# Kernel tuning notes

Hardware: AMD Instinct MI355X
Metric: run time of the kernel (lower is better)

The kernel has to match this reference:

```python
import jax, jax.numpy as jnp
import numpy as np

N0, T0, T1 = 3514368, 135168, 12288   # hop-0 nodes, layer-0 targets, layer-1 targets
F0, F1 = 25, 10                        # sampled fanouts per layer
D, H, C = 100, 256, 128                # in_feat, hidden, class_count
IC = 4096                              # id_count (src/pos/neg each)


def setup_inputs() -> dict:
    key = jax.random.key(0)
    ks = jax.random.split(key, 16)

    def w(k, shape):
        return jax.random.normal(k, shape, dtype=jnp.float32) * (1.0 / np.sqrt(shape[0]))

    x_feat = jax.random.normal(ks[0], (N0, D), dtype=jnp.float32)
    col_ind0 = jax.random.randint(ks[1], (T0, F0), 0, N0)
    col_ind1 = jax.random.randint(ks[2], (T1, F1), 0, T0)
    reverse_map = jax.random.randint(ks[3], (3 * IC,), 0, T1)

    return {
        "x_feat": x_feat,
        "Wn0": w(ks[4], (D, H)), "Ws0": w(ks[5], (D, H)), "b0": jnp.zeros((H,), jnp.float32),
        "Wn1": w(ks[6], (H, C)), "Ws1": w(ks[7], (H, C)), "b1": jnp.zeros((C,), jnp.float32),
        "Wp1": w(ks[8], (C, C)), "bp1": jnp.zeros((C,), jnp.float32),
        "Wp2": w(ks[9], (C, 1)), "bp2": jnp.zeros((1,), jnp.float32),
        "col_ind0": col_ind0, "col_ind1": col_ind1, "reverse_map": reverse_map,
        "id_count": IC,
    }


def reference(x_feat, Wn0, Ws0, b0, Wn1, Ws1, b1, Wp1, bp1, Wp2, bp2,
              col_ind0, col_ind1, reverse_map, id_count):
    t0 = col_ind0.shape[0]
    t1 = col_ind1.shape[0]

    # SAGEConv layer 0 (mean aggregator): gather neighbor feats, mean over fanout
    neigh0 = x_feat[col_ind0].mean(axis=1)                    # [t0, D]
    h = neigh0 @ Wn0 + x_feat[:t0] @ Ws0 + b0                 # [t0, H]
    h = jax.nn.relu(h)                                        # dropout p=0 (eval)

    # SAGEConv layer 1 -> class_count, no activation on final layer
    neigh1 = h[col_ind1].mean(axis=1)                         # [t1, H]
    out_unique = neigh1 @ Wn1 + h[:t1] @ Ws1 + b1             # [t1, C]

    # embedding gather of unique outputs back to (src, pos_dst, neg_dst) order
    out_feat = out_unique[reverse_map]                        # [3*ic, C]
    src = out_feat[:id_count]
    pos = out_feat[id_count:2 * id_count]
    neg = out_feat[2 * id_count:3 * id_count]

    h_src = jnp.concatenate([src, src], axis=0)               # [2*ic, C]
    h_dst = jnp.concatenate([pos, neg], axis=0)               # [2*ic, C]

    # edge predictor: MLP on elementwise product -> scalar score
    e = h_src * h_dst
    scores = jax.nn.relu(e @ Wp1 + bp1) @ Wp2 + bp2           # [2*ic, 1]
    return scores
```

## Files before the change

kernel.cpp:

```cpp
#include <hip/hip_runtime.h>
#include <hip/hip_bf16.h>

#define N0_ 3514368
#define T0_ 135168
#define T1_ 12288
#define F0_ 25
#define F1_ 10
#define D_  100
#define H_  256
#define C_  128
#define IC_ 4096


typedef __attribute__((ext_vector_type(8))) short bf8_t;
typedef __attribute__((ext_vector_type(4))) float f4_t;

__device__ inline void split_bf16(float v, ushort& hi, ushort& lo) {
    __hip_bfloat16 hb = __float2bfloat16(v);
    float hf = __bfloat162float(hb);
    __hip_bfloat16 lb = __float2bfloat16(v - hf);
    hi = *reinterpret_cast<ushort*>(&hb);
    lo = *reinterpret_cast<ushort*>(&lb);
}

__global__ __launch_bounds__(256) void bz_zero(unsigned int* __restrict__ flag32) {
    const int i = blockIdx.x * 256 + threadIdx.x;
    if (i < T0_ / 4) flag32[i] = 0u;
}

__global__ __launch_bounds__(256) void bs_set(const int* __restrict__ col1,
                                              unsigned char* __restrict__ flag) {
    const int i = blockIdx.x * 256 + threadIdx.x;
    if (i < T1_ * F1_) flag[col1[i]] = 1;
    if (i < T1_) flag[i] = 1;
}

__global__ __launch_bounds__(256) void k0_packW(const float* __restrict__ Wn0,
                                                const float* __restrict__ Ws0,
                                                ushort* __restrict__ Wpk) {
    const int nb = blockIdx.x;
    for (int it = 0; it < 4; ++it) {
        const int task = threadIdx.x + it * 256;
        const int ks   = task >> 7;
        const int part = (task >> 6) & 1;
        const int lane = task & 63;
        const int n  = nb * 16 + (lane & 15);
        const int kb = (ks & 3) * 32 + (lane >> 4) * 8;
        const float* src = (ks < 4) ? Wn0 : Ws0;
        ushort out[8];
#pragma unroll
        for (int j = 0; j < 8; ++j) {
            const int k = kb + j;
            float v = (k < D_) ? src[k * H_ + n] : 0.f;
            ushort hi, lo;
            split_bf16(v, hi, lo);
            out[j] = part ? lo : hi;
        }
        ushort* dst = Wpk + ((size_t)((nb * 8 + ks) * 2 + part) * 64 + lane) * 8;
        *reinterpret_cast<bf8_t*>(dst) = *reinterpret_cast<bf8_t*>(out);
    }
}

__global__ __launch_bounds__(256) void k12_fused(const float* __restrict__ xf,
                                                 const int* __restrict__ col0,
                                                 const ushort* __restrict__ Wpk,
                                                 const float* __restrict__ b0,
                                                 const unsigned char* __restrict__ flag,
                                                 float* __restrict__ h) {
    __shared__ ushort Afr[4][8][2][512];
    const int lane = threadIdx.x & 63;
    const int wid  = threadIdx.x >> 6;
    const int r    = lane & 15;
    const int kg   = lane >> 4;
    const size_t row = (size_t)blockIdx.x * 64 + wid * 16 + r;
    const bool needed = (flag[row] != 0);

    float accN[4][8];
    float accS[4][8];
#pragma unroll
    for (int ks = 0; ks < 4; ++ks)
#pragma unroll
        for (int j = 0; j < 8; ++j) { accN[ks][j] = 0.f; accS[ks][j] = 0.f; }

    if (needed) {
        const int* cp = col0 + row * F0_;
#pragma unroll 5
        for (int jn = 0; jn < F0_; ++jn) {
            const float* rp = xf + (size_t)cp[jn] * D_;
#pragma unroll
            for (int ks = 0; ks < 3; ++ks) {
                float4 a = *reinterpret_cast<const float4*>(rp + ks * 32 + kg * 8);
                float4 b = *reinterpret_cast<const float4*>(rp + ks * 32 + kg * 8 + 4);
                accN[ks][0] += a.x; accN[ks][1] += a.y; accN[ks][2] += a.z; accN[ks][3] += a.w;
                accN[ks][4] += b.x; accN[ks][5] += b.y; accN[ks][6] += b.z; accN[ks][7] += b.w;
            }
            if (kg == 0) {
                float4 a = *reinterpret_cast<const float4*>(rp + 96);
                accN[3][0] += a.x; accN[3][1] += a.y; accN[3][2] += a.z; accN[3][3] += a.w;
            }
        }
        const float* rp = xf + row * D_;
#pragma unroll
        for (int ks = 0; ks < 3; ++ks) {
            float4 a = *reinterpret_cast<const float4*>(rp + ks * 32 + kg * 8);
            float4 b = *reinterpret_cast<const float4*>(rp + ks * 32 + kg * 8 + 4);
            accS[ks][0] = a.x; accS[ks][1] = a.y; accS[ks][2] = a.z; accS[ks][3] = a.w;
            accS[ks][4] = b.x; accS[ks][5] = b.y; accS[ks][6] = b.z; accS[ks][7] = b.w;
        }
        if (kg == 0) {
            float4 a = *reinterpret_cast<const float4*>(rp + 96);
            accS[3][0] = a.x; accS[3][1] = a.y; accS[3][2] = a.z; accS[3][3] = a.w;
        }
    }

    const float inv = 1.0f / F0_;
#pragma unroll
    for (int ks = 0; ks < 4; ++ks) {
        bf8_t hN, lN, hS, lS;
#pragma unroll
        for (int j = 0; j < 8; ++j) {
            ushort hi, lo;
            split_bf16(accN[ks][j] * inv, hi, lo);
            hN[j] = (short)hi; lN[j] = (short)lo;
            split_bf16(accS[ks][j], hi, lo);
            hS[j] = (short)hi; lS[j] = (short)lo;
        }
        *reinterpret_cast<bf8_t*>(&Afr[wid][ks    ][0][lane * 8]) = hN;
        *reinterpret_cast<bf8_t*>(&Afr[wid][ks    ][1][lane * 8]) = lN;
        *reinterpret_cast<bf8_t*>(&Afr[wid][ks + 4][0][lane * 8]) = hS;
        *reinterpret_cast<bf8_t*>(&Afr[wid][ks + 4][1][lane * 8]) = lS;
    }
    __syncthreads();

    const int nb0 = wid * 4;
    f4_t acc[4][4] = {};
#pragma unroll
    for (int ks = 0; ks < 8; ++ks) {
        bf8_t ah[4], al[4], bh[4], bl[4];
#pragma unroll
        for (int rb = 0; rb < 4; ++rb) {
            ah[rb] = *reinterpret_cast<const bf8_t*>(&Afr[rb][ks][0][lane * 8]);
            al[rb] = *reinterpret_cast<const bf8_t*>(&Afr[rb][ks][1][lane * 8]);
        }
#pragma unroll
        for (int ci = 0; ci < 4; ++ci) {
            const ushort* p = Wpk + ((size_t)(((nb0 + ci) * 8 + ks) * 2) * 64 + lane) * 8;
            bh[ci] = *reinterpret_cast<const bf8_t*>(p);
            bl[ci] = *reinterpret_cast<const bf8_t*>(p + 512);
        }
#pragma unroll
        for (int rb = 0; rb < 4; ++rb)
#pragma unroll
            for (int ci = 0; ci < 4; ++ci) {
                acc[rb][ci] = __builtin_amdgcn_mfma_f32_16x16x32_bf16(ah[rb], bh[ci], acc[rb][ci], 0, 0, 0);
                acc[rb][ci] = __builtin_amdgcn_mfma_f32_16x16x32_bf16(ah[rb], bl[ci], acc[rb][ci], 0, 0, 0);
                acc[rb][ci] = __builtin_amdgcn_mfma_f32_16x16x32_bf16(al[rb], bh[ci], acc[rb][ci], 0, 0, 0);
            }
    }

    const int col_in = lane & 15;
    const int rgrp   = lane >> 4;
    bool vflag[4][4];
#pragma unroll
    for (int rb = 0; rb < 4; ++rb)
#pragma unroll
        for (int q = 0; q < 4; ++q)
            vflag[rb][q] = (flag[(size_t)blockIdx.x * 64 + rb * 16 + rgrp * 4 + q] != 0);
#pragma unroll
    for (int ci = 0; ci < 4; ++ci) {
        const int n = (nb0 + ci) * 16 + col_in;
        const float bias = b0[n];
#pragma unroll
        for (int rb = 0; rb < 4; ++rb) {
            const size_t rowb = (size_t)blockIdx.x * 64 + rb * 16 + rgrp * 4;
#pragma unroll
            for (int q = 0; q < 4; ++q) {
                if (vflag[rb][q]) {
                    float v = acc[rb][ci][q] + bias;
                    h[(rowb + q) * H_ + n] = v > 0.f ? v : 0.f;
                }
            }
        }
    }
}

__global__ __launch_bounds__(256) void k3_layer1(const float* __restrict__ h,
                                                 const int* __restrict__ col1,
                                                 const float* __restrict__ Wn1,
                                                 const float* __restrict__ Ws1,
                                                 const float* __restrict__ b1,
                                                 float* __restrict__ out_u) {
    __shared__ __align__(16) float Ng[16 * H_];
    __shared__ __align__(16) float Sf[16 * H_];
    const int t = threadIdx.x;
    const int base = blockIdx.x * 16;

    for (int r = 0; r < 16; ++r) {
        float a = 0.f;
#pragma unroll
        for (int j = 0; j < F1_; ++j) {
            int idx = col1[(base + r) * F1_ + j];
            a += h[(size_t)idx * H_ + t];
        }
        Ng[r * H_ + t] = a * (1.0f / F1_);
        Sf[r * H_ + t] = h[(size_t)(base + r) * H_ + t];
    }
    __syncthreads();

    const int c  = t & (C_ - 1);
    const int rg = t >> 7;
    float acc[8];
    const float bias = b1[c];
#pragma unroll
    for (int r8 = 0; r8 < 8; ++r8) acc[r8] = bias;

    for (int d4 = 0; d4 < H_ / 4; ++d4) {
        const int d = d4 * 4;
        const float wn0_ = Wn1[(d + 0) * C_ + c];
        const float wn1_ = Wn1[(d + 1) * C_ + c];
        const float wn2_ = Wn1[(d + 2) * C_ + c];
        const float wn3_ = Wn1[(d + 3) * C_ + c];
        const float ws0_ = Ws1[(d + 0) * C_ + c];
        const float ws1_ = Ws1[(d + 1) * C_ + c];
        const float ws2_ = Ws1[(d + 2) * C_ + c];
        const float ws3_ = Ws1[(d + 3) * C_ + c];
#pragma unroll
        for (int r8 = 0; r8 < 8; ++r8) {
            const int r = rg * 8 + r8;
            float4 n = *reinterpret_cast<const float4*>(&Ng[r * H_ + d]);
            float4 s = *reinterpret_cast<const float4*>(&Sf[r * H_ + d]);
            acc[r8] += n.x * wn0_ + n.y * wn1_ + n.z * wn2_ + n.w * wn3_
                     + s.x * ws0_ + s.y * ws1_ + s.z * ws2_ + s.w * ws3_;
        }
    }
#pragma unroll
    for (int r8 = 0; r8 < 8; ++r8)
        out_u[(size_t)(base + rg * 8 + r8) * C_ + c] = acc[r8];
}

__global__ __launch_bounds__(256) void k4_edges(const float* __restrict__ out_u,
                                                const int* __restrict__ rmap,
                                                const float* __restrict__ Wp1,
                                                const float* __restrict__ bp1,
                                                const float* __restrict__ Wp2,
                                                const float* __restrict__ bp2,
                                                float* __restrict__ scores) {
    __shared__ __align__(16) float E[32 * C_];
    const int t = threadIdx.x;
    const int base = blockIdx.x * 32;
    const int f = t & 127;
    const int half = t >> 7;

    for (int rr = 0; rr < 16; ++rr) {
        const int row = rr * 2 + half;
        const int j = base + row;
        const int si = rmap[j & (IC_ - 1)];
        const int di = rmap[IC_ + j];
        E[row * C_ + f] = out_u[(size_t)si * C_ + f] * out_u[(size_t)di * C_ + f];
    }
    __syncthreads();

    float acc[16];
    const float bias = bp1[f];
#pragma unroll
    for (int r16 = 0; r16 < 16; ++r16) acc[r16] = bias;

    for (int d4 = 0; d4 < C_ / 4; ++d4) {
        const int d = d4 * 4;
        const float w0 = Wp1[(d + 0) * C_ + f];
        const float w1 = Wp1[(d + 1) * C_ + f];
        const float w2 = Wp1[(d + 2) * C_ + f];
        const float w3 = Wp1[(d + 3) * C_ + f];
#pragma unroll
        for (int r16 = 0; r16 < 16; ++r16) {
            const int r = half * 16 + r16;
            float4 e4 = *reinterpret_cast<const float4*>(&E[r * C_ + d]);
            acc[r16] += e4.x * w0 + e4.y * w1 + e4.z * w2 + e4.w * w3;
        }
    }
    __syncthreads();
#pragma unroll
    for (int r16 = 0; r16 < 16; ++r16) {
        float v = acc[r16];
        E[(half * 16 + r16) * C_ + f] = v > 0.f ? v : 0.f;
    }
    __syncthreads();

    const int r = t >> 3;
    const int s = t & 7;
    float p = 0.f;
#pragma unroll
    for (int k4 = 0; k4 < 4; ++k4) {
        float4 tv = *reinterpret_cast<const float4*>(&E[r * C_ + s * 16 + k4 * 4]);
        float4 wv = *reinterpret_cast<const float4*>(&Wp2[s * 16 + k4 * 4]);
        p += tv.x * wv.x + tv.y * wv.y + tv.z * wv.z + tv.w * wv.w;
    }
    p += __shfl_down(p, 4, 8);
    p += __shfl_down(p, 2, 8);
    p += __shfl_down(p, 1, 8);
    if (s == 0) scores[base + r] = p + bp2[0];
}

extern "C" void kernel_launch(void* const* d_in, const int* in_sizes, int n_in,
                              void* d_out, int out_size, void* d_ws, size_t ws_size,
                              hipStream_t stream) {
    const float* xf   = (const float*)d_in[0];
    const float* Wn0  = (const float*)d_in[1];
    const float* Ws0  = (const float*)d_in[2];
    const float* b0   = (const float*)d_in[3];
    const float* Wn1  = (const float*)d_in[4];
    const float* Ws1  = (const float*)d_in[5];
    const float* b1   = (const float*)d_in[6];
    const float* Wp1  = (const float*)d_in[7];
    const float* bp1  = (const float*)d_in[8];
    const float* Wp2  = (const float*)d_in[9];
    const float* bp2  = (const float*)d_in[10];
    const int*   col0 = (const int*)d_in[11];
    const int*   col1 = (const int*)d_in[12];
    const int*   rmap = (const int*)d_in[13];

    char* ws = (char*)d_ws;
    float*  h     = (float*)ws;
    float*  out_u = h + (size_t)T0_ * H_;
    ushort* Wpk   = (ushort*)(out_u + (size_t)T1_ * C_);
    unsigned char* flag = (unsigned char*)(Wpk + (size_t)16 * 8 * 2 * 64 * 8);
    float*  scores = (float*)d_out;

    hipLaunchKernelGGL(bz_zero, dim3((T0_ / 4 + 255) / 256), dim3(256), 0, stream,
                       (unsigned int*)flag);
    hipLaunchKernelGGL(bs_set, dim3((T1_ * F1_ + 255) / 256), dim3(256), 0, stream,
                       col1, flag);
    hipLaunchKernelGGL(k0_packW, dim3(16), dim3(256), 0, stream, Wn0, Ws0, Wpk);
    hipLaunchKernelGGL(k12_fused, dim3(T0_ / 64), dim3(256), 0, stream,
                       xf, col0, Wpk, b0, flag, h);
    hipLaunchKernelGGL(k3_layer1, dim3(T1_ / 16), dim3(256), 0, stream,
                       h, col1, Wn1, Ws1, b1, out_u);
    hipLaunchKernelGGL(k4_edges, dim3((2 * IC_) / 32), dim3(256), 0, stream,
                       out_u, rmap, Wp1, bp1, Wp2, bp2, scores);
}
```

Before: 402.0 us.

## Keep A fragments in registers and loop each wave over all output columns

Drops the shared-memory staging of the bf16 hi/lo A fragments and the block-wide barrier. Each wave now multiplies its own 16 rows against all 16 column blocks of the packed weight, instead of sharing A across waves and computing only 4 column blocks. This removes LDS traffic and the __syncthreads. In exchange, each wave reads four times as much packed weight data from global memory/cache, and the MFMA chain per accumulator is serial with less independent work in flight.

Result: slower. 475.1 us (+18.2%).

```diff
diff --git a/kernel.cpp b/kernel.cpp
--- a/kernel.cpp
+++ b/kernel.cpp
@@ -67,7 +67,6 @@
                                                  const float* __restrict__ b0,
                                                  const unsigned char* __restrict__ flag,
                                                  float* __restrict__ h) {
-    __shared__ ushort Afr[4][8][2][512];
     const int lane = threadIdx.x & 63;
     const int wid  = threadIdx.x >> 6;
     const int r    = lane & 15;
@@ -113,6 +112,7 @@
         }
     }
 
+    bf8_t afH[8], afL[8];
     const float inv = 1.0f / F0_;
 #pragma unroll
     for (int ks = 0; ks < 4; ++ks) {
@@ -125,60 +125,37 @@
             split_bf16(accS[ks][j], hi, lo);
             hS[j] = (short)hi; lS[j] = (short)lo;
         }
-        *reinterpret_cast<bf8_t*>(&Afr[wid][ks    ][0][lane * 8]) = hN;
-        *reinterpret_cast<bf8_t*>(&Afr[wid][ks    ][1][lane * 8]) = lN;
-        *reinterpret_cast<bf8_t*>(&Afr[wid][ks + 4][0][lane * 8]) = hS;
-        *reinterpret_cast<bf8_t*>(&Afr[wid][ks + 4][1][lane * 8]) = lS;
-    }
-    __syncthreads();
-
-    const int nb0 = wid * 4;
-    f4_t acc[4][4] = {};
-#pragma unroll
-    for (int ks = 0; ks < 8; ++ks) {
-        bf8_t ah[4], al[4], bh[4], bl[4];
-#pragma unroll
-        for (int rb = 0; rb < 4; ++rb) {
-            ah[rb] = *reinterpret_cast<const bf8_t*>(&Afr[rb][ks][0][lane * 8]);
-            al[rb] = *reinterpret_cast<const bf8_t*>(&Afr[rb][ks][1][lane * 8]);
-        }
-#pragma unroll
-        for (int ci = 0; ci < 4; ++ci) {
-            const ushort* p = Wpk + ((size_t)(((nb0 + ci) * 8 + ks) * 2) * 64 + lane) * 8;
-            bh[ci] = *reinterpret_cast<const bf8_t*>(p);
-            bl[ci] = *reinterpret_cast<const bf8_t*>(p + 512);
-        }
-#pragma unroll
-        for (int rb = 0; rb < 4; ++rb)
-#pragma unroll
-            for (int ci = 0; ci < 4; ++ci) {
-                acc[rb][ci] = __builtin_amdgcn_mfma_f32_16x16x32_bf16(ah[rb], bh[ci], acc[rb][ci], 0, 0, 0);
-                acc[rb][ci] = __builtin_amdgcn_mfma_f32_16x16x32_bf16(ah[rb], bl[ci], acc[rb][ci], 0, 0, 0);
-                acc[rb][ci] = __builtin_amdgcn_mfma_f32_16x16x32_bf16(al[rb], bh[ci], acc[rb][ci], 0, 0, 0);
-            }
-    }
-
+        afH[ks] = hN; afL[ks] = lN;
+        afH[ks + 4] = hS; afL[ks + 4] = lS;
+    }
+
+    const int rgrp = lane >> 4;
+    bool vflag[4];
+#pragma unroll
+    for (int q = 0; q < 4; ++q)
+        vflag[q] = (flag[(size_t)blockIdx.x * 64 + wid * 16 + rgrp * 4 + q] != 0);
+    const size_t rowb = (size_t)blockIdx.x * 64 + wid * 16 + rgrp * 4;
     const int col_in = lane & 15;
-    const int rgrp   = lane >> 4;
-    bool vflag[4][4];
-#pragma unroll
-    for (int rb = 0; rb < 4; ++rb)
-#pragma unroll
-        for (int q = 0; q < 4; ++q)
-            vflag[rb][q] = (flag[(size_t)blockIdx.x * 64 + rb * 16 + rgrp * 4 + q] != 0);
-#pragma unroll
-    for (int ci = 0; ci < 4; ++ci) {
-        const int n = (nb0 + ci) * 16 + col_in;
+
+#pragma unroll 4
+    for (int nb = 0; nb < 16; ++nb) {
+        f4_t acc = {};
+#pragma unroll
+        for (int ks = 0; ks < 8; ++ks) {
+            const ushort* p = Wpk + ((size_t)((nb * 8 + ks) * 2) * 64 + lane) * 8;
+            bf8_t bh = *reinterpret_cast<const bf8_t*>(p);
+            bf8_t bl = *reinterpret_cast<const bf8_t*>(p + 512);
+            acc = __builtin_amdgcn_mfma_f32_16x16x32_bf16(afH[ks], bh, acc, 0, 0, 0);
+            acc = __builtin_amdgcn_mfma_f32_16x16x32_bf16(afH[ks], bl, acc, 0, 0, 0);
+            acc = __builtin_amdgcn_mfma_f32_16x16x32_bf16(afL[ks], bh, acc, 0, 0, 0);
+        }
+        const int n = nb * 16 + col_in;
         const float bias = b0[n];
 #pragma unroll
-        for (int rb = 0; rb < 4; ++rb) {
-            const size_t rowb = (size_t)blockIdx.x * 64 + rb * 16 + rgrp * 4;
-#pragma unroll
-            for (int q = 0; q < 4; ++q) {
-                if (vflag[rb][q]) {
-                    float v = acc[rb][ci][q] + bias;
-                    h[(rowb + q) * H_ + n] = v > 0.f ? v : 0.f;
-                }
+        for (int q = 0; q < 4; ++q) {
+            if (vflag[q]) {
+                float v = acc[q] + bias;
+                h[(rowb + q) * H_ + n] = v > 0.f ? v : 0.f;
             }
         }
     }
```

## Compact needed layer-0 rows into a list and launch work only for them

Applied to the files above, without the earlier changes.

Adds count/scan/emit kernels that build a compacted list of the layer-0 rows actually referenced by layer 1, and rewrites the fused layer-0 kernel to process rows from this list. Blocks past the count exit early, so unneeded rows no longer occupy MFMA or block slots. Neighbor indices are also preloaded into registers. It adds three small kernel launches, including a serial single-thread scan, and turns the output stores into scattered writes.

Measured after the change: 394.7 us. About the same (-1.8%).

```diff
diff --git a/kernel.cpp b/kernel.cpp
--- a/kernel.cpp
+++ b/kernel.cpp
@@ -10,6 +10,7 @@
 #define H_  256
 #define C_  128
 #define IC_ 4096
+#define CBLK_ 132
 
 
 typedef __attribute__((ext_vector_type(8))) short bf8_t;
@@ -33,6 +34,51 @@
     const int i = blockIdx.x * 256 + threadIdx.x;
     if (i < T1_ * F1_) flag[col1[i]] = 1;
     if (i < T1_) flag[i] = 1;
+}
+
+__global__ __launch_bounds__(1024) void kc_count(const unsigned char* __restrict__ flag,
+                                                 int* __restrict__ counts) {
+    __shared__ int wsum[16];
+    const int i = blockIdx.x * 1024 + threadIdx.x;
+    const int pred = flag[i] ? 1 : 0;
+    unsigned long long b = __ballot(pred);
+    const int lane = threadIdx.x & 63, w = threadIdx.x >> 6;
+    if (lane == 0) wsum[w] = __popcll(b);
+    __syncthreads();
+    if (threadIdx.x == 0) {
+        int s = 0;
+        for (int k = 0; k < 16; ++k) s += wsum[k];
+        counts[blockIdx.x] = s;
+    }
+}
+
+__global__ void kc_scan(const int* __restrict__ counts,
+                        int* __restrict__ offs, int* __restrict__ ntot) {
+    if (threadIdx.x == 0 && blockIdx.x == 0) {
+        int s = 0;
+        for (int k = 0; k < CBLK_; ++k) { offs[k] = s; s += counts[k]; }
+        ntot[0] = s;
+    }
+}
+
+__global__ __launch_bounds__(1024) void kc_emit(const unsigned char* __restrict__ flag,
+                                                const int* __restrict__ offs,
+                                                int* __restrict__ rowlist) {
+    __shared__ int wsum[16];
+    __shared__ int woff[16];
+    const int i = blockIdx.x * 1024 + threadIdx.x;
+    const int pred = flag[i] ? 1 : 0;
+    unsigned long long b = __ballot(pred);
+    const int lane = threadIdx.x & 63, w = threadIdx.x >> 6;
+    const int lanepre = __popcll(b & ((1ULL << lane) - 1ULL));
+    if (lane == 0) wsum[w] = __popcll(b);
+    __syncthreads();
+    if (threadIdx.x == 0) {
+        int s = 0;
+        for (int k = 0; k < 16; ++k) { woff[k] = s; s += wsum[k]; }
+    }
+    __syncthreads();
+    if (pred) rowlist[offs[blockIdx.x] + woff[w] + lanepre] = i;
 }
 
 __global__ __launch_bounds__(256) void k0_packW(const float* __restrict__ Wn0,
@@ -65,15 +111,26 @@
                                                  const int* __restrict__ col0,
                                                  const ushort* __restrict__ Wpk,
                                                  const float* __restrict__ b0,
-                                                 const unsigned char* __restrict__ flag,
+                                                 const int* __restrict__ rowlist,
+                                                 const int* __restrict__ ntot,
                                                  float* __restrict__ h) {
     __shared__ ushort Afr[4][8][2][512];
+    __shared__ int rl[64];
+    const int n = ntot[0];
+    if (blockIdx.x * 64 >= n) return;
+
     const int lane = threadIdx.x & 63;
     const int wid  = threadIdx.x >> 6;
     const int r    = lane & 15;
     const int kg   = lane >> 4;
-    const size_t row = (size_t)blockIdx.x * 64 + wid * 16 + r;
-    const bool needed = (flag[row] != 0);
+    const int cidx = blockIdx.x * 64 + wid * 16 + r;
+    const bool act = (cidx < n);
+    const int orow = rowlist[act ? cidx : 0];
+
+    if (threadIdx.x < 64) {
+        const int c2 = blockIdx.x * 64 + threadIdx.x;
+        rl[threadIdx.x] = (c2 < n) ? rowlist[c2] : -1;
+    }
 
     float accN[4][8];
     float accS[4][8];
@@ -82,11 +139,14 @@
 #pragma unroll
         for (int j = 0; j < 8; ++j) { accN[ks][j] = 0.f; accS[ks][j] = 0.f; }
 
-    if (needed) {
-        const int* cp = col0 + row * F0_;
+    if (act) {
+        const int* cp = col0 + (size_t)orow * F0_;
+        int idxs[F0_];
+#pragma unroll
+        for (int j = 0; j < F0_; ++j) idxs[j] = cp[j];
 #pragma unroll 5
         for (int jn = 0; jn < F0_; ++jn) {
-            const float* rp = xf + (size_t)cp[jn] * D_;
+            const float* rp = xf + (size_t)idxs[jn] * D_;
 #pragma unroll
             for (int ks = 0; ks < 3; ++ks) {
                 float4 a = *reinterpret_cast<const float4*>(rp + ks * 32 + kg * 8);
@@ -99,7 +159,7 @@
                 accN[3][0] += a.x; accN[3][1] += a.y; accN[3][2] += a.z; accN[3][3] += a.w;
             }
         }
-        const float* rp = xf + row * D_;
+        const float* rp = xf + (size_t)orow * D_;
 #pragma unroll
         for (int ks = 0; ks < 3; ++ks) {
             float4 a = *reinterpret_cast<const float4*>(rp + ks * 32 + kg * 8);
@@ -160,24 +220,24 @@
 
     const int col_in = lane & 15;
     const int rgrp   = lane >> 4;
-    bool vflag[4][4];
+    int orows[4][4];
 #pragma unroll
     for (int rb = 0; rb < 4; ++rb)
 #pragma unroll
         for (int q = 0; q < 4; ++q)
-            vflag[rb][q] = (flag[(size_t)blockIdx.x * 64 + rb * 16 + rgrp * 4 + q] != 0);
+            orows[rb][q] = rl[rb * 16 + rgrp * 4 + q];
 #pragma unroll
     for (int ci = 0; ci < 4; ++ci) {
-        const int n = (nb0 + ci) * 16 + col_in;
-        const float bias = b0[n];
+        const int nn = (nb0 + ci) * 16 + col_in;
+        const float bias = b0[nn];
 #pragma unroll
         for (int rb = 0; rb < 4; ++rb) {
-            const size_t rowb = (size_t)blockIdx.x * 64 + rb * 16 + rgrp * 4;
 #pragma unroll
             for (int q = 0; q < 4; ++q) {
-                if (vflag[rb][q]) {
+                const int o = orows[rb][q];
+                if (o >= 0) {
                     float v = acc[rb][ci][q] + bias;
-                    h[(rowb + q) * H_ + n] = v > 0.f ? v : 0.f;
+                    h[(size_t)o * H_ + nn] = v > 0.f ? v : 0.f;
                 }
             }
         }
@@ -324,15 +384,22 @@
     float*  out_u = h + (size_t)T0_ * H_;
     ushort* Wpk   = (ushort*)(out_u + (size_t)T1_ * C_);
     unsigned char* flag = (unsigned char*)(Wpk + (size_t)16 * 8 * 2 * 64 * 8);
-    float*  scores = (float*)d_out;
+    int*    counts  = (int*)(flag + T0_);
+    int*    offs    = counts + CBLK_;
+    int*    ntot    = offs + CBLK_;
+    int*    rowlist = ntot + 1;
+    float*  scores  = (float*)d_out;
 
     hipLaunchKernelGGL(bz_zero, dim3((T0_ / 4 + 255) / 256), dim3(256), 0, stream,
                        (unsigned int*)flag);
     hipLaunchKernelGGL(bs_set, dim3((T1_ * F1_ + 255) / 256), dim3(256), 0, stream,
                        col1, flag);
+    hipLaunchKernelGGL(kc_count, dim3(CBLK_), dim3(1024), 0, stream, flag, counts);
+    hipLaunchKernelGGL(kc_scan, dim3(1), dim3(64), 0, stream, counts, offs, ntot);
+    hipLaunchKernelGGL(kc_emit, dim3(CBLK_), dim3(1024), 0, stream, flag, offs, rowlist);
     hipLaunchKernelGGL(k0_packW, dim3(16), dim3(256), 0, stream, Wn0, Ws0, Wpk);
     hipLaunchKernelGGL(k12_fused, dim3(T0_ / 64), dim3(256), 0, stream,
-                       xf, col0, Wpk, b0, flag, h);
+                       xf, col0, Wpk, b0, rowlist, ntot, h);
     hipLaunchKernelGGL(k3_layer1, dim3(T1_ / 16), dim3(256), 0, stream,
                        h, col1, Wn1, Ws1, b1, out_u);
     hipLaunchKernelGGL(k4_edges, dim3((2 * IC_) / 32), dim3(256), 0, stream,
```
